# Kernel optimization log

Hardware: AMD Instinct MI355X
Metric: run time of the kernel (lower is better)

The kernel has to match this reference:

```python
import jax, jax.numpy as jnp
import numpy as np

C = 256      # channel_num
K = 9        # key_num
B, H, W = 8, 64, 64


def setup_inputs() -> dict:
    key = jax.random.key(0)
    ks = jax.random.split(key, 12)
    s = 1.0 / np.sqrt(C)
    return {
        "query_layer": jax.random.normal(ks[0], (B, C, H, W), jnp.float32),
        "key_layer": jax.random.normal(ks[1], (B, C, H, W), jnp.float32),
        "gumbel_noise": jax.random.gumbel(ks[2], (B, K, H, W), jnp.float32),
        "w_refer": jax.random.normal(ks[3], (C, C), jnp.float32) * s,
        "b_refer": jax.random.normal(ks[4], (C,), jnp.float32) * 0.01,
        "w_attn": jax.random.normal(ks[5], (K, C), jnp.float32) * s,
        "b_attn": jax.random.normal(ks[6], (K,), jnp.float32) * 0.01,
        "w_mask": jax.random.normal(ks[7], (K, C), jnp.float32) * s,
        "b_mask": jax.random.normal(ks[8], (K,), jnp.float32) * 0.01,
        "w_off": jax.random.normal(ks[9], (2 * K, C), jnp.float32) * 0.02,
        "b_off": jax.random.normal(ks[10], (2 * K,), jnp.float32) * 0.01,
        "temp": 1,
    }


def _conv1x1(w, b, x):
    # w: (O,C), x: (B,C,H,W) -> (B,O,H,W)
    return jnp.einsum('oc,bchw->bohw', w, x) + b[None, :, None, None]


def _sample_one(img, py, px):
    # img: (C,H,W); py,px: (K,H,W) absolute sampling coords (bilinear, zero pad)
    h, w = img.shape[1], img.shape[2]
    y0 = jnp.floor(py)
    x0 = jnp.floor(px)
    wy = py - y0          # weight toward y0+1
    wx = px - x0

    def gather(yi, xi):
        valid = (yi >= 0) & (yi < h) & (xi >= 0) & (xi < w)
        yc = jnp.clip(yi, 0, h - 1).astype(jnp.int32)
        xc = jnp.clip(xi, 0, w - 1).astype(jnp.int32)
        return img[:, yc, xc] * valid[None].astype(img.dtype)  # (C,K,H,W)

    out = (gather(y0, x0) * ((1 - wy) * (1 - wx))[None]
           + gather(y0, x0 + 1) * ((1 - wy) * wx)[None]
           + gather(y0 + 1, x0) * (wy * (1 - wx))[None]
           + gather(y0 + 1, x0 + 1) * (wy * wx)[None])
    return out  # (C,K,H,W)


def reference(query_layer, key_layer, gumbel_noise, w_refer, b_refer,
              w_attn, b_attn, w_mask, b_mask, w_off, b_off, temp):
    key_feature = _conv1x1(w_refer, b_refer, key_layer)          # (B,C,H,W)
    attn_weights = _conv1x1(w_attn, b_attn, query_layer)         # (B,K,H,W)
    soft_mask = _conv1x1(w_mask, b_mask, query_layer)            # (B,K,H,W)
    # gumbel_softmax(hard=False) over key dim
    hard_mask = jax.nn.softmax((soft_mask + gumbel_noise) / temp, axis=1)
    offset = _conv1x1(w_off, b_off, query_layer)                 # (B,2K,H,W)

    # faithful to offset[:, i:i+2]: overlapping (dy,dx) slices
    dy = offset[:, 0:K]        # (B,K,H,W)
    dx = offset[:, 1:K + 1]    # (B,K,H,W)
    ys = jnp.arange(H, dtype=offset.dtype)[None, None, :, None]
    xs = jnp.arange(W, dtype=offset.dtype)[None, None, None, :]
    py = ys + dy
    px = xs + dx

    sampled = jax.vmap(_sample_one)(key_feature, py, px)         # (B,C,K,H,W)

    aw = jax.nn.softmax(attn_weights * hard_mask, axis=1)        # (B,K,H,W)
    out = jnp.einsum('bkhw,bckhw->bchw', aw, sampled)            # (B,C,H,W)
    return out
```

## Files before the change

### kernel.cpp

```cpp
#include <hip/hip_runtime.h>

typedef unsigned short u16;
typedef __attribute__((ext_vector_type(8))) short bf16x8;
typedef __attribute__((ext_vector_type(4))) float f32x4;

__device__ __forceinline__ u16 f2bf(float f) {
    unsigned u = __float_as_uint(f);
    unsigned r = (u + 0x7fffu + ((u >> 16) & 1u)) >> 16;
    return (u16)r;
}
__device__ __forceinline__ float bf2f(u16 h) {
    union { unsigned u; float f; } x; x.u = ((unsigned)h) << 16; return x.f;
}

#define NB 8
#define NC 256
#define NK 9
#define NH 64
#define NW 64
#define NP 4096
#define BAND 320
#define SB_STRIDE 328

__global__ __launch_bounds__(256) void kf_gemm(const float* __restrict__ key,
                                               const float* __restrict__ w_refer,
                                               const float* __restrict__ b_refer,
                                               u16* __restrict__ kf16)
{
    const int pt  = blockIdx.x;
    const int b   = pt >> 5;
    const int p0  = (pt & 31) << 7;
    const int co0 = blockIdx.y << 7;
    const int lane = threadIdx.x & 63, wid = threadIdx.x >> 6;
    const int wm = wid & 1, wn = wid >> 1;
    const int fr = lane & 15, kq = (lane >> 4) << 3;

    f32x4 acc[4][4];
    #pragma unroll
    for (int i = 0; i < 4; ++i)
        #pragma unroll
        for (int j = 0; j < 4; ++j) acc[i][j] = (f32x4){0.f, 0.f, 0.f, 0.f};

    for (int ks = 0; ks < 8; ++ks) {
        const int k0 = (ks << 5) + kq;
        bf16x8 af[4], bfv[4];
        #pragma unroll
        for (int mi = 0; mi < 4; ++mi) {
            const float* src = &w_refer[(size_t)(co0 + (wm << 6) + (mi << 4) + fr) * NC + k0];
            float4 v0 = *(const float4*)src;
            float4 v1 = *(const float4*)(src + 4);
            bf16x8 a;
            a[0] = (short)f2bf(v0.x); a[1] = (short)f2bf(v0.y);
            a[2] = (short)f2bf(v0.z); a[3] = (short)f2bf(v0.w);
            a[4] = (short)f2bf(v1.x); a[5] = (short)f2bf(v1.y);
            a[6] = (short)f2bf(v1.z); a[7] = (short)f2bf(v1.w);
            af[mi] = a;
        }
        #pragma unroll
        for (int ni = 0; ni < 4; ++ni) {
            const float* src = &key[((size_t)b * NC + k0) * NP + p0 + (wn << 6) + (ni << 4) + fr];
            bf16x8 bv;
            #pragma unroll
            for (int j = 0; j < 8; ++j) bv[j] = (short)f2bf(src[(size_t)j * NP]);
            bfv[ni] = bv;
        }
        #pragma unroll
        for (int mi = 0; mi < 4; ++mi)
            #pragma unroll
            for (int ni = 0; ni < 4; ++ni)
                acc[mi][ni] = __builtin_amdgcn_mfma_f32_16x16x32_bf16(af[mi], bfv[ni], acc[mi][ni], 0, 0, 0);
    }
    const int col = lane & 15, rbase = (lane >> 4) << 2;
    #pragma unroll
    for (int mi = 0; mi < 4; ++mi) {
        #pragma unroll
        for (int rr = 0; rr < 4; ++rr) {
            int co = co0 + (wm << 6) + (mi << 4) + rbase + rr;
            float bias = b_refer[co];
            u16* dst = &kf16[((size_t)b * NC + co) * NP + p0 + (wn << 6) + col];
            #pragma unroll
            for (int ni = 0; ni < 4; ++ni)
                dst[ni << 4] = f2bf(acc[mi][ni][rr] + bias);
        }
    }
}

__global__ __launch_bounds__(256) void hd_gemm(const float* __restrict__ query,
                                               const float* __restrict__ w_attn, const float* __restrict__ b_attn,
                                               const float* __restrict__ w_mask, const float* __restrict__ b_mask,
                                               const float* __restrict__ w_off,  const float* __restrict__ b_off,
                                               float* __restrict__ hd)
{
    __shared__ u16 A[48][264];
    const int pt = blockIdx.x;
    const int b  = pt >> 5;
    const int p0 = (pt & 31) << 7;
    const int t = threadIdx.x;
    const int lane = t & 63, wn = t >> 6;
    const int fr = lane & 15, kq = (lane >> 4) << 3;

    for (int i = t; i < 1152; i += 256) {
        int o = i >> 5, c = (i & 31) << 3;
        const float* src = (o < 9) ? &w_attn[o * NC + c]
                       : (o < 18 ? &w_mask[(o - 9) * NC + c]
                                 : &w_off[(o - 18) * NC + c]);
        float4 v0 = *(const float4*)src;
        float4 v1 = *(const float4*)(src + 4);
        bf16x8 a;
        a[0] = (short)f2bf(v0.x); a[1] = (short)f2bf(v0.y);
        a[2] = (short)f2bf(v0.z); a[3] = (short)f2bf(v0.w);
        a[4] = (short)f2bf(v1.x); a[5] = (short)f2bf(v1.y);
        a[6] = (short)f2bf(v1.z); a[7] = (short)f2bf(v1.w);
        *(bf16x8*)&A[o][c] = a;
    }
    for (int i = t; i < 384; i += 256) {
        bf16x8 z = {0,0,0,0,0,0,0,0};
        *(bf16x8*)&A[36 + (i >> 5)][(i & 31) << 3] = z;
    }
    __syncthreads();

    f32x4 acc[3][2];
    #pragma unroll
    for (int i = 0; i < 3; ++i)
        #pragma unroll
        for (int j = 0; j < 2; ++j) acc[i][j] = (f32x4){0.f, 0.f, 0.f, 0.f};

    for (int ks = 0; ks < 8; ++ks) {
        const int k0 = (ks << 5) + kq;
        bf16x8 af[3], bfv[2];
        #pragma unroll
        for (int mi = 0; mi < 3; ++mi)
            af[mi] = *(const bf16x8*)&A[(mi << 4) + fr][k0];
        #pragma unroll
        for (int ni = 0; ni < 2; ++ni) {
            const float* src = &query[((size_t)b * NC + k0) * NP + p0 + (wn << 5) + (ni << 4) + fr];
            bf16x8 bv;
            #pragma unroll
            for (int j = 0; j < 8; ++j) bv[j] = (short)f2bf(src[(size_t)j * NP]);
            bfv[ni] = bv;
        }
        #pragma unroll
        for (int mi = 0; mi < 3; ++mi)
            #pragma unroll
            for (int ni = 0; ni < 2; ++ni)
                acc[mi][ni] = __builtin_amdgcn_mfma_f32_16x16x32_bf16(af[mi], bfv[ni], acc[mi][ni], 0, 0, 0);
    }
    const int col = lane & 15, rbase = (lane >> 4) << 2;
    #pragma unroll
    for (int mi = 0; mi < 3; ++mi) {
        #pragma unroll
        for (int rr = 0; rr < 4; ++rr) {
            int co = (mi << 4) + rbase + rr;
            if (co < 36) {
                float bias = (co < 9) ? b_attn[co] : (co < 18) ? b_mask[co - 9] : b_off[co - 18];
                #pragma unroll
                for (int ni = 0; ni < 2; ++ni)
                    hd[(size_t)co * (NB * NP) + (size_t)b * NP + p0 + (wn << 5) + (ni << 4) + col]
                        = acc[mi][ni][rr] + bias;
            }
        }
    }
}

__global__ __launch_bounds__(128) void meta_pass(const float* __restrict__ hd,
                                                 const float* __restrict__ gumbel,
                                                 const int* __restrict__ temp_p,
                                                 float4* __restrict__ wgt, uint2* __restrict__ offs)
{
    const int gp = blockIdx.x * 128 + threadIdx.x;
    const int b = gp >> 12, pxl = gp & 4095;
    const int row = pxl >> 6, xcol = pxl & 63;

    float v[36];
    #pragma unroll
    for (int o = 0; o < 36; ++o) v[o] = hd[(size_t)o * (NB * NP) + gp];

    int ti = temp_p[0];
    float tempf = (ti >= 1 && ti < (1 << 23)) ? (float)ti : __int_as_float(ti);
    float am[9], hs[9];
    float mx = -1e30f;
    #pragma unroll
    for (int k = 0; k < 9; ++k) {
        am[k] = v[k];
        float g = gumbel[((size_t)b * NK + k) * NP + pxl];
        hs[k] = (v[9 + k] + g) / tempf;
        mx = fmaxf(mx, hs[k]);
    }
    float ssum = 0.f;
    #pragma unroll
    for (int k = 0; k < 9; ++k) { hs[k] = __expf(hs[k] - mx); ssum += hs[k]; }
    float inv = 1.f / ssum;
    float lg[9]; float mx2 = -1e30f;
    #pragma unroll
    for (int k = 0; k < 9; ++k) { lg[k] = am[k] * (hs[k] * inv); mx2 = fmaxf(mx2, lg[k]); }
    float s2 = 0.f;
    #pragma unroll
    for (int k = 0; k < 9; ++k) { lg[k] = __expf(lg[k] - mx2); s2 += lg[k]; }
    float inv2 = 1.f / s2;
    #pragma unroll
    for (int k = 0; k < 9; ++k) {
        float a = lg[k] * inv2;
        float pyv = (float)row  + v[18 + k];
        float pxv = (float)xcol + v[19 + k];
        float y0f = floorf(pyv), x0f = floorf(pxv);
        float wy = pyv - y0f, wx = pxv - x0f;
        int y0 = (int)y0f, x0 = (int)x0f;
        int y1 = y0 + 1, x1 = x0 + 1;
        float vy0 = (y0 >= 0 && y0 < NH) ? 1.f : 0.f;
        float vy1 = (y1 >= 0 && y1 < NH) ? 1.f : 0.f;
        float vx0 = (x0 >= 0 && x0 < NW) ? 1.f : 0.f;
        float vx1 = (x1 >= 0 && x1 < NW) ? 1.f : 0.f;
        int y0c = min(max(y0, 0), NH - 1), y1c = min(max(y1, 0), NH - 1);
        int x0c = min(max(x0, 0), NW - 1), x1c = min(max(x1, 0), NW - 1);
        unsigned o00 = (unsigned)(y0c * NW + x0c), o01 = (unsigned)(y0c * NW + x1c);
        unsigned o10 = (unsigned)(y1c * NW + x0c), o11 = (unsigned)(y1c * NW + x1c);
        size_t idx = ((size_t)b * NK + k) * NP + pxl;
        wgt[idx]  = make_float4(a * (1.f - wy) * (1.f - wx) * vy0 * vx0,
                                a * (1.f - wy) * wx * vy0 * vx1,
                                a * wy * (1.f - wx) * vy1 * vx0,
                                a * wy * wx * vy1 * vx1);
        offs[idx] = make_uint2(o00 | (o01 << 16), o10 | (o11 << 16));
    }
}

__global__ __launch_bounds__(512, 4) void sample_pass(const u16* __restrict__ kf16,
                                                      const float4* __restrict__ wgt,
                                                      const uint2* __restrict__ offs,
                                                      float* __restrict__ out)
{
    __shared__ float Sf[64][BAND];

    const int bid = blockIdx.x;
    const int b = bid & 7, row = bid >> 3;
    const int t = threadIdx.x;
    const int lane = t & 63, wid = t >> 6;
    const int fr = lane & 15, kq = (lane >> 4) << 3;
    const int c0 = wid << 5;
    const int ylo = min(max(row - 2, 0), NH - 5);
    const int base = ylo << 6;
    const u16* kfb = kf16 + (size_t)b * NC * NP + base;

    const int px = t & 63, kg = t >> 6;
    size_t idx0 = ((size_t)b * NK + kg) * NP + (row << 6) + px;
    float4 wv0 = wgt[idx0];
    uint2  ov0 = offs[idx0];
    float4 wv1 = make_float4(0.f, 0.f, 0.f, 0.f);
    uint2  ov1 = make_uint2(0u, 0u);
    if (kg == 0) {
        size_t idx1 = ((size_t)b * NK + 8) * NP + (row << 6) + px;
        wv1 = wgt[idx1]; ov1 = offs[idx1];
    }
    bf16x8 apre[4][2];
    #pragma unroll
    for (int s = 0; s < 4; ++s)
        #pragma unroll
        for (int mi = 0; mi < 2; ++mi)
            apre[s][mi] = *(const bf16x8*)&kfb[(size_t)(c0 + (mi << 4) + fr) * NP + (s << 5) + kq];

    #pragma unroll
    for (int i = 0; i < 10; ++i)
        ((float4*)Sf)[t + (i << 9)] = (float4){0.f, 0.f, 0.f, 0.f};
    __syncthreads();

    bool esc = false;
    {
        #pragma unroll
        for (int s = 0; s < 2; ++s) {
            if (s == 1 && kg != 0) break;
            float4 wv = s ? wv1 : wv0;
            uint2  ov = s ? ov1 : ov0;
            int   o4[4] = { (int)(ov.x & 0xffffu), (int)(ov.x >> 16),
                            (int)(ov.y & 0xffffu), (int)(ov.y >> 16) };
            float w4[4] = { wv.x, wv.y, wv.z, wv.w };
            #pragma unroll
            for (int c = 0; c < 4; ++c) {
                int u = o4[c] - base;
                if ((unsigned)u < (unsigned)BAND) atomicAdd(&Sf[px][u], w4[c]);
                else esc = true;
            }
        }
    }
    __syncthreads();

    u16* Sb = (u16*)&Sf[0][0];
    bf16x8 pk[5];
    int pp[5], pj[5];
    #pragma unroll
    for (int r = 0; r < 5; ++r) {
        int i = t + (r << 9);
        int p = i / 40, j = (i % 40) << 3;
        float4 a = *(const float4*)&Sf[p][j];
        float4 c = *(const float4*)&Sf[p][j + 4];
        bf16x8 q;
        q[0] = (short)f2bf(a.x); q[1] = (short)f2bf(a.y);
        q[2] = (short)f2bf(a.z); q[3] = (short)f2bf(a.w);
        q[4] = (short)f2bf(c.x); q[5] = (short)f2bf(c.y);
        q[6] = (short)f2bf(c.z); q[7] = (short)f2bf(c.w);
        pk[r] = q; pp[r] = p; pj[r] = j;
    }
    __syncthreads();
    #pragma unroll
    for (int r = 0; r < 5; ++r)
        *(bf16x8*)&Sb[pp[r] * SB_STRIDE + pj[r]] = pk[r];
    __syncthreads();

    f32x4 acc[2][4];
    #pragma unroll
    for (int i = 0; i < 2; ++i)
        #pragma unroll
        for (int j = 0; j < 4; ++j) acc[i][j] = (f32x4){0.f, 0.f, 0.f, 0.f};

    #pragma unroll
    for (int step = 0; step < 10; ++step) {
        bf16x8 a0 = apre[step & 3][0], a1 = apre[step & 3][1];
        if (step + 4 < 10) {
            #pragma unroll
            for (int mi = 0; mi < 2; ++mi)
                apre[step & 3][mi] =
                    *(const bf16x8*)&kfb[(size_t)(c0 + (mi << 4) + fr) * NP + ((step + 4) << 5) + kq];
        }
        bf16x8 bfv[4];
        #pragma unroll
        for (int ni = 0; ni < 4; ++ni)
            bfv[ni] = *(const bf16x8*)&Sb[((ni << 4) + fr) * SB_STRIDE + (step << 5) + kq];
        #pragma unroll
        for (int ni = 0; ni < 4; ++ni) {
            acc[0][ni] = __builtin_amdgcn_mfma_f32_16x16x32_bf16(a0, bfv[ni], acc[0][ni], 0, 0, 0);
            acc[1][ni] = __builtin_amdgcn_mfma_f32_16x16x32_bf16(a1, bfv[ni], acc[1][ni], 0, 0, 0);
        }
    }

    const int col = lane & 15, rbase = (lane >> 4) << 2;
    float* ob = out + (size_t)b * NC * NP + (row << 6);
    #pragma unroll
    for (int mi = 0; mi < 2; ++mi) {
        #pragma unroll
        for (int rr = 0; rr < 4; ++rr) {
            int c = c0 + (mi << 4) + rbase + rr;
            #pragma unroll
            for (int ni = 0; ni < 4; ++ni)
                ob[(size_t)c * NP + (ni << 4) + col] = acc[mi][ni][rr];
        }
    }

    __syncthreads();
    if (esc) {
        for (int s = 0; s < (kg == 0 ? 2 : 1); ++s) {
            int k = s ? 8 : kg;
            size_t idx = ((size_t)b * NK + k) * NP + (row << 6) + px;
            float4 wv = wgt[idx];
            uint2  ov = offs[idx];
            int   o4[4] = { (int)(ov.x & 0xffffu), (int)(ov.x >> 16),
                            (int)(ov.y & 0xffffu), (int)(ov.y >> 16) };
            float w4[4] = { wv.x, wv.y, wv.z, wv.w };
            for (int c = 0; c < 4; ++c) {
                int u = o4[c] - base;
                if ((unsigned)u >= (unsigned)BAND) {
                    for (int cc = 0; cc < NC; ++cc)
                        atomicAdd(&ob[(size_t)cc * NP + px],
                                  w4[c] * bf2f(kf16[((size_t)b * NC + cc) * NP + o4[c]]));
                }
            }
        }
    }
}

extern "C" void kernel_launch(void* const* d_in, const int* in_sizes, int n_in,
                              void* d_out, int out_size, void* d_ws, size_t ws_size,
                              hipStream_t stream)
{
    const float* query   = (const float*)d_in[0];
    const float* key     = (const float*)d_in[1];
    const float* gumbel  = (const float*)d_in[2];
    const float* w_refer = (const float*)d_in[3];
    const float* b_refer = (const float*)d_in[4];
    const float* w_attn  = (const float*)d_in[5];
    const float* b_attn  = (const float*)d_in[6];
    const float* w_mask  = (const float*)d_in[7];
    const float* b_mask  = (const float*)d_in[8];
    const float* w_off   = (const float*)d_in[9];
    const float* b_off   = (const float*)d_in[10];
    const int*   temp    = (const int*)d_in[11];
    float* out = (float*)d_out;

    u16*    kf16 = (u16*)d_ws;
    float4* wgt  = (float4*)((char*)d_ws + (size_t)NB * NP * NC * 2);
    uint2*  offs = (uint2*)((char*)wgt + (size_t)NB * NK * NP * 16);
    float*  hd   = (float*)((char*)offs + (size_t)NB * NK * NP * 8);

    kf_gemm<<<dim3(256, 2), 256, 0, stream>>>(key, w_refer, b_refer, kf16);
    hd_gemm<<<256, 256, 0, stream>>>(query, w_attn, b_attn, w_mask, b_mask, w_off, b_off, hd);
    meta_pass<<<256, 128, 0, stream>>>(hd, gumbel, temp, wgt, offs);
    sample_pass<<<NB * NH, 512, 0, stream>>>(kf16, wgt, offs, out);
}
```

Measured before the change: 65.38 us.

## Stage key tile in LDS for kf_gemm and fuse head GEMM with meta pass

kf_gemm now loads a 64-pixel by 256-channel key tile into shared memory once with coalesced float4 reads. It then computes all 256 output channels per block, instead of doing strided scalar loads per wave. The head GEMM and the meta/softmax pass are fused through a shared-memory transpose, which removes the hd intermediate buffer and one kernel launch. In sample_pass the scatter now runs before the A-fragment prefetch, and the bf16 repack puts a barrier inside the loop. That barrier adds synchronisation in exchange for fewer registers.

```diff
diff --git a/kernel.cpp b/kernel.cpp
--- a/kernel.cpp
+++ b/kernel.cpp
@@ -21,19 +21,32 @@
 #define NP 4096
 #define BAND 320
 #define SB_STRIDE 328
+#define KS_STRIDE 264
 
 __global__ __launch_bounds__(256) void kf_gemm(const float* __restrict__ key,
                                                const float* __restrict__ w_refer,
                                                const float* __restrict__ b_refer,
                                                u16* __restrict__ kf16)
 {
-    const int pt  = blockIdx.x;
-    const int b   = pt >> 5;
-    const int p0  = (pt & 31) << 7;
-    const int co0 = blockIdx.y << 7;
-    const int lane = threadIdx.x & 63, wid = threadIdx.x >> 6;
-    const int wm = wid & 1, wn = wid >> 1;
+    __shared__ u16 K_s[64 * KS_STRIDE];
+    const int bid = blockIdx.x;
+    const int b   = bid >> 6;
+    const int p0  = (bid & 63) << 6;
+    const int t = threadIdx.x;
+    const int lane = t & 63, wid = t >> 6;
     const int fr = lane & 15, kq = (lane >> 4) << 3;
+    const int co0w = wid << 6;
+
+    #pragma unroll
+    for (int rep = 0; rep < 16; ++rep) {
+        int k = (rep << 4) + (t >> 4), px4 = (t & 15) << 2;
+        float4 v = *(const float4*)&key[((size_t)b * NC + k) * NP + p0 + px4];
+        K_s[(px4 + 0) * KS_STRIDE + k] = f2bf(v.x);
+        K_s[(px4 + 1) * KS_STRIDE + k] = f2bf(v.y);
+        K_s[(px4 + 2) * KS_STRIDE + k] = f2bf(v.z);
+        K_s[(px4 + 3) * KS_STRIDE + k] = f2bf(v.w);
+    }
+    __syncthreads();
 
     f32x4 acc[4][4];
     #pragma unroll
@@ -46,7 +59,7 @@
         bf16x8 af[4], bfv[4];
         #pragma unroll
         for (int mi = 0; mi < 4; ++mi) {
-            const float* src = &w_refer[(size_t)(co0 + (wm << 6) + (mi << 4) + fr) * NC + k0];
+            const float* src = &w_refer[(size_t)(co0w + (mi << 4) + fr) * NC + k0];
             float4 v0 = *(const float4*)src;
             float4 v1 = *(const float4*)(src + 4);
             bf16x8 a;
@@ -57,13 +70,8 @@
             af[mi] = a;
         }
         #pragma unroll
-        for (int ni = 0; ni < 4; ++ni) {
-            const float* src = &key[((size_t)b * NC + k0) * NP + p0 + (wn << 6) + (ni << 4) + fr];
-            bf16x8 bv;
-            #pragma unroll
-            for (int j = 0; j < 8; ++j) bv[j] = (short)f2bf(src[(size_t)j * NP]);
-            bfv[ni] = bv;
-        }
+        for (int ni = 0; ni < 4; ++ni)
+            bfv[ni] = *(const bf16x8*)&K_s[((ni << 4) + fr) * KS_STRIDE + k0];
         #pragma unroll
         for (int mi = 0; mi < 4; ++mi)
             #pragma unroll
@@ -75,9 +83,9 @@
     for (int mi = 0; mi < 4; ++mi) {
         #pragma unroll
         for (int rr = 0; rr < 4; ++rr) {
-            int co = co0 + (wm << 6) + (mi << 4) + rbase + rr;
+            int co = co0w + (mi << 4) + rbase + rr;
             float bias = b_refer[co];
-            u16* dst = &kf16[((size_t)b * NC + co) * NP + p0 + (wn << 6) + col];
+            u16* dst = &kf16[((size_t)b * NC + co) * NP + p0 + col];
             #pragma unroll
             for (int ni = 0; ni < 4; ++ni)
                 dst[ni << 4] = f2bf(acc[mi][ni][rr] + bias);
@@ -85,13 +93,16 @@
     }
 }
 
-__global__ __launch_bounds__(256) void hd_gemm(const float* __restrict__ query,
-                                               const float* __restrict__ w_attn, const float* __restrict__ b_attn,
-                                               const float* __restrict__ w_mask, const float* __restrict__ b_mask,
-                                               const float* __restrict__ w_off,  const float* __restrict__ b_off,
-                                               float* __restrict__ hd)
+__global__ __launch_bounds__(256) void head_meta(const float* __restrict__ query,
+                                                 const float* __restrict__ gumbel,
+                                                 const float* __restrict__ w_attn, const float* __restrict__ b_attn,
+                                                 const float* __restrict__ w_mask, const float* __restrict__ b_mask,
+                                                 const float* __restrict__ w_off,  const float* __restrict__ b_off,
+                                                 const int* __restrict__ temp_p,
+                                                 float4* __restrict__ wgt, uint2* __restrict__ offs)
 {
     __shared__ u16 A[48][264];
+    __shared__ float hdT[128][41];
     const int pt = blockIdx.x;
     const int b  = pt >> 5;
     const int p0 = (pt & 31) << 7;
@@ -150,76 +161,70 @@
     for (int mi = 0; mi < 3; ++mi) {
         #pragma unroll
         for (int rr = 0; rr < 4; ++rr) {
-            int co = (mi << 4) + rbase + rr;
-            if (co < 36) {
-                float bias = (co < 9) ? b_attn[co] : (co < 18) ? b_mask[co - 9] : b_off[co - 18];
+            int o = (mi << 4) + rbase + rr;
+            if (o < 36) {
+                float bias = (o < 9) ? b_attn[o] : (o < 18) ? b_mask[o - 9] : b_off[o - 18];
                 #pragma unroll
                 for (int ni = 0; ni < 2; ++ni)
-                    hd[(size_t)co * (NB * NP) + (size_t)b * NP + p0 + (wn << 5) + (ni << 4) + col]
-                        = acc[mi][ni][rr] + bias;
+                    hdT[(wn << 5) + (ni << 4) + col][o] = acc[mi][ni][rr] + bias;
             }
         }
     }
-}
-
-__global__ __launch_bounds__(128) void meta_pass(const float* __restrict__ hd,
-                                                 const float* __restrict__ gumbel,
-                                                 const int* __restrict__ temp_p,
-                                                 float4* __restrict__ wgt, uint2* __restrict__ offs)
-{
-    const int gp = blockIdx.x * 128 + threadIdx.x;
-    const int b = gp >> 12, pxl = gp & 4095;
-    const int row = pxl >> 6, xcol = pxl & 63;
-
-    float v[36];
-    #pragma unroll
-    for (int o = 0; o < 36; ++o) v[o] = hd[(size_t)o * (NB * NP) + gp];
-
-    int ti = temp_p[0];
-    float tempf = (ti >= 1 && ti < (1 << 23)) ? (float)ti : __int_as_float(ti);
-    float am[9], hs[9];
-    float mx = -1e30f;
-    #pragma unroll
-    for (int k = 0; k < 9; ++k) {
-        am[k] = v[k];
-        float g = gumbel[((size_t)b * NK + k) * NP + pxl];
-        hs[k] = (v[9 + k] + g) / tempf;
-        mx = fmaxf(mx, hs[k]);
-    }
-    float ssum = 0.f;
-    #pragma unroll
-    for (int k = 0; k < 9; ++k) { hs[k] = __expf(hs[k] - mx); ssum += hs[k]; }
-    float inv = 1.f / ssum;
-    float lg[9]; float mx2 = -1e30f;
-    #pragma unroll
-    for (int k = 0; k < 9; ++k) { lg[k] = am[k] * (hs[k] * inv); mx2 = fmaxf(mx2, lg[k]); }
-    float s2 = 0.f;
-    #pragma unroll
-    for (int k = 0; k < 9; ++k) { lg[k] = __expf(lg[k] - mx2); s2 += lg[k]; }
-    float inv2 = 1.f / s2;
-    #pragma unroll
-    for (int k = 0; k < 9; ++k) {
-        float a = lg[k] * inv2;
-        float pyv = (float)row  + v[18 + k];
-        float pxv = (float)xcol + v[19 + k];
-        float y0f = floorf(pyv), x0f = floorf(pxv);
-        float wy = pyv - y0f, wx = pxv - x0f;
-        int y0 = (int)y0f, x0 = (int)x0f;
-        int y1 = y0 + 1, x1 = x0 + 1;
-        float vy0 = (y0 >= 0 && y0 < NH) ? 1.f : 0.f;
-        float vy1 = (y1 >= 0 && y1 < NH) ? 1.f : 0.f;
-        float vx0 = (x0 >= 0 && x0 < NW) ? 1.f : 0.f;
-        float vx1 = (x1 >= 0 && x1 < NW) ? 1.f : 0.f;
-        int y0c = min(max(y0, 0), NH - 1), y1c = min(max(y1, 0), NH - 1);
-        int x0c = min(max(x0, 0), NW - 1), x1c = min(max(x1, 0), NW - 1);
-        unsigned o00 = (unsigned)(y0c * NW + x0c), o01 = (unsigned)(y0c * NW + x1c);
-        unsigned o10 = (unsigned)(y1c * NW + x0c), o11 = (unsigned)(y1c * NW + x1c);
-        size_t idx = ((size_t)b * NK + k) * NP + pxl;
-        wgt[idx]  = make_float4(a * (1.f - wy) * (1.f - wx) * vy0 * vx0,
-                                a * (1.f - wy) * wx * vy0 * vx1,
-                                a * wy * (1.f - wx) * vy1 * vx0,
-                                a * wy * wx * vy1 * vx1);
-        offs[idx] = make_uint2(o00 | (o01 << 16), o10 | (o11 << 16));
+    __syncthreads();
+
+    if (t < 128) {
+        const int pxg = p0 + t;
+        const int row = pxg >> 6, xcol = pxg & 63;
+        float v[36];
+        #pragma unroll
+        for (int o = 0; o < 36; ++o) v[o] = hdT[t][o];
+
+        int ti = temp_p[0];
+        float tempf = (ti >= 1 && ti < (1 << 23)) ? (float)ti : __int_as_float(ti);
+        float am[9], hs[9];
+        float mx = -1e30f;
+        #pragma unroll
+        for (int k = 0; k < 9; ++k) {
+            am[k] = v[k];
+            float g = gumbel[((size_t)b * NK + k) * NP + pxg];
+            hs[k] = (v[9 + k] + g) / tempf;
+            mx = fmaxf(mx, hs[k]);
+        }
+        float ssum = 0.f;
+        #pragma unroll
+        for (int k = 0; k < 9; ++k) { hs[k] = __expf(hs[k] - mx); ssum += hs[k]; }
+        float inv = 1.f / ssum;
+        float lg[9]; float mx2 = -1e30f;
+        #pragma unroll
+        for (int k = 0; k < 9; ++k) { lg[k] = am[k] * (hs[k] * inv); mx2 = fmaxf(mx2, lg[k]); }
+        float s2 = 0.f;
+        #pragma unroll
+        for (int k = 0; k < 9; ++k) { lg[k] = __expf(lg[k] - mx2); s2 += lg[k]; }
+        float inv2 = 1.f / s2;
+        #pragma unroll
+        for (int k = 0; k < 9; ++k) {
+            float a = lg[k] * inv2;
+            float pyv = (float)row  + v[18 + k];
+            float pxv = (float)xcol + v[19 + k];
+            float y0f = floorf(pyv), x0f = floorf(pxv);
+            float wy = pyv - y0f, wx = pxv - x0f;
+            int y0 = (int)y0f, x0 = (int)x0f;
+            int y1 = y0 + 1, x1 = x0 + 1;
+            float vy0 = (y0 >= 0 && y0 < NH) ? 1.f : 0.f;
+            float vy1 = (y1 >= 0 && y1 < NH) ? 1.f : 0.f;
+            float vx0 = (x0 >= 0 && x0 < NW) ? 1.f : 0.f;
+            float vx1 = (x1 >= 0 && x1 < NW) ? 1.f : 0.f;
+            int y0c = min(max(y0, 0), NH - 1), y1c = min(max(y1, 0), NH - 1);
+            int x0c = min(max(x0, 0), NW - 1), x1c = min(max(x1, 0), NW - 1);
+            unsigned o00 = (unsigned)(y0c * NW + x0c), o01 = (unsigned)(y0c * NW + x1c);
+            unsigned o10 = (unsigned)(y1c * NW + x0c), o11 = (unsigned)(y1c * NW + x1c);
+            size_t idx = ((size_t)b * NK + k) * NP + pxg;
+            wgt[idx]  = make_float4(a * (1.f - wy) * (1.f - wx) * vy0 * vx0,
+                                    a * (1.f - wy) * wx * vy0 * vx1,
+                                    a * wy * (1.f - wx) * vy1 * vx0,
+                                    a * wy * wx * vy1 * vx1);
+            offs[idx] = make_uint2(o00 | (o01 << 16), o10 | (o11 << 16));
+        }
     }
 }
 
@@ -250,6 +255,30 @@
         size_t idx1 = ((size_t)b * NK + 8) * NP + (row << 6) + px;
         wv1 = wgt[idx1]; ov1 = offs[idx1];
     }
+
+    #pragma unroll
+    for (int i = 0; i < 10; ++i)
+        ((float4*)Sf)[t + (i << 9)] = (float4){0.f, 0.f, 0.f, 0.f};
+    __syncthreads();
+
+    bool esc = false;
+    #pragma unroll
+    for (int s = 0; s < 2; ++s) {
+        if (s == 1 && kg != 0) break;
+        float4 wv = s ? wv1 : wv0;
+        uint2  ov = s ? ov1 : ov0;
+        int   o4[4] = { (int)(ov.x & 0xffffu), (int)(ov.x >> 16),
+                        (int)(ov.y & 0xffffu), (int)(ov.y >> 16) };
+        float w4[4] = { wv.x, wv.y, wv.z, wv.w };
+        #pragma unroll
+        for (int c = 0; c < 4; ++c) {
+            int u = o4[c] - base;
+            if ((unsigned)u < (unsigned)BAND) atomicAdd(&Sf[px][u], w4[c]);
+            else esc = true;
+        }
+    }
+    __syncthreads();
+
     bf16x8 apre[4][2];
     #pragma unroll
     for (int s = 0; s < 4; ++s)
@@ -257,34 +286,7 @@
         for (int mi = 0; mi < 2; ++mi)
             apre[s][mi] = *(const bf16x8*)&kfb[(size_t)(c0 + (mi << 4) + fr) * NP + (s << 5) + kq];
 
-    #pragma unroll
-    for (int i = 0; i < 10; ++i)
-        ((float4*)Sf)[t + (i << 9)] = (float4){0.f, 0.f, 0.f, 0.f};
-    __syncthreads();
-
-    bool esc = false;
-    {
-        #pragma unroll
-        for (int s = 0; s < 2; ++s) {
-            if (s == 1 && kg != 0) break;
-            float4 wv = s ? wv1 : wv0;
-            uint2  ov = s ? ov1 : ov0;
-            int   o4[4] = { (int)(ov.x & 0xffffu), (int)(ov.x >> 16),
-                            (int)(ov.y & 0xffffu), (int)(ov.y >> 16) };
-            float w4[4] = { wv.x, wv.y, wv.z, wv.w };
-            #pragma unroll
-            for (int c = 0; c < 4; ++c) {
-                int u = o4[c] - base;
-                if ((unsigned)u < (unsigned)BAND) atomicAdd(&Sf[px][u], w4[c]);
-                else esc = true;
-            }
-        }
-    }
-    __syncthreads();
-
     u16* Sb = (u16*)&Sf[0][0];
-    bf16x8 pk[5];
-    int pp[5], pj[5];
     #pragma unroll
     for (int r = 0; r < 5; ++r) {
         int i = t + (r << 9);
@@ -296,12 +298,9 @@
         q[2] = (short)f2bf(a.z); q[3] = (short)f2bf(a.w);
         q[4] = (short)f2bf(c.x); q[5] = (short)f2bf(c.y);
         q[6] = (short)f2bf(c.z); q[7] = (short)f2bf(c.w);
-        pk[r] = q; pp[r] = p; pj[r] = j;
-    }
-    __syncthreads();
-    #pragma unroll
-    for (int r = 0; r < 5; ++r)
-        *(bf16x8*)&Sb[pp[r] * SB_STRIDE + pj[r]] = pk[r];
+        __syncthreads();
+        *(bf16x8*)&Sb[p * SB_STRIDE + j] = q;
+    }
     __syncthreads();
 
     f32x4 acc[2][4];
@@ -386,10 +385,9 @@
     u16*    kf16 = (u16*)d_ws;
     float4* wgt  = (float4*)((char*)d_ws + (size_t)NB * NP * NC * 2);
     uint2*  offs = (uint2*)((char*)wgt + (size_t)NB * NK * NP * 16);
-    float*  hd   = (float*)((char*)offs + (size_t)NB * NK * NP * 8);
-
-    kf_gemm<<<dim3(256, 2), 256, 0, stream>>>(key, w_refer, b_refer, kf16);
-    hd_gemm<<<256, 256, 0, stream>>>(query, w_attn, b_attn, w_mask, b_mask, w_off, b_off, hd);
-    meta_pass<<<256, 128, 0, stream>>>(hd, gumbel, temp, wgt, offs);
-    sample_pass<<<NB * NH, 512, 0, stream>>>(kf16, wgt, offs, out);
-}
+
+    kf_gemm<<<512, 256, 0, stream>>>(key, w_refer, b_refer, kf16);
+    head_meta<<<256, 256, 0, stream>>>(query, gumbel, w_attn, b_attn, w_mask, b_mask,
+                                       w_off, b_off, temp, wgt, offs);
+    sample_pass<<<512, 512, 0, stream>>>(kf16, wgt, offs, out);
+}
```

Result: faster. 62.10 us (-5.0%).
